# Optimization experiments

Hardware: AMD Instinct MI355X
Metric: run time of the kernel (lower is better)

## Reference

```python
import jax, jax.numpy as jnp
import numpy as np

N = 100000   # nodes
E = 1200000  # edges
C = 64       # in_channels
H = 64       # hidden_channels
OUT = 10     # out_channels
G = 128      # graphs in batch
L = 3        # num_conv_layers
EPS = 1e-5   # BatchNorm eps


def batchnorm(x, g, b):
    # training-mode BatchNorm1d: biased batch stats over the node/graph axis
    mu = x.mean(axis=0)
    var = x.var(axis=0)
    return (x - mu) * jax.lax.rsqrt(var + EPS) * g + b


def _gcn_norm(edge_index):
    # add self-loops (weight 1) then symmetric normalization deg^-1/2 * w * deg^-1/2
    loop = jnp.arange(N)
    src = jnp.concatenate([edge_index[0], loop])
    dst = jnp.concatenate([edge_index[1], loop])
    w = jnp.ones((E + N,), jnp.float32)
    deg = jax.ops.segment_sum(w, src, num_segments=N)
    dis = jnp.where(deg > 0, jax.lax.rsqrt(deg), 0.0)
    norm = dis[src] * w * dis[dst]
    return src, dst, norm


def gcn_conv(h, W, b, src, dst, norm):
    # linear transform -> gather source features -> edge-normalize -> scatter-add to dst
    hw = h @ W
    msg = norm[:, None] * hw[src]          # [E+N, H]
    return jax.ops.segment_sum(msg, dst, num_segments=N) + b


def setup_inputs() -> dict:
    key = jax.random.key(0)
    ks = jax.random.split(key, 8)
    s = 0.1
    return {
        'x': jax.random.normal(ks[0], (N, C), jnp.float32),
        'edge_index': jax.random.randint(ks[1], (2, E), 0, N),
        'batch_idx': jnp.sort(jax.random.randint(ks[2], (N,), 0, G)),
        # BN params initialized as in the module: weight=1, bias=1e-4
        'bn_feat_g': jnp.ones((C,), jnp.float32),
        'bn_feat_b': jnp.full((C,), 1e-4, jnp.float32),
        'W_feat': jax.random.normal(ks[3], (C, H), jnp.float32) * s,  # conv_feat (gfn=True -> pure linear)
        'b_feat': jnp.zeros((H,), jnp.float32),
        'conv_bn_g': jnp.ones((L, H), jnp.float32),
        'conv_bn_b': jnp.full((L, H), 1e-4, jnp.float32),
        'conv_W': jax.random.normal(ks[4], (L, H, H), jnp.float32) * s,
        'conv_b': jnp.zeros((L, H), jnp.float32),
        'bn_fc_g': jnp.ones((H,), jnp.float32),
        'bn_fc_b': jnp.full((H,), 1e-4, jnp.float32),
        'W_fc': jax.random.normal(ks[5], (H, H), jnp.float32) * s,
        'b_fc': jnp.zeros((H,), jnp.float32),
        'bn_hid_g': jnp.ones((H,), jnp.float32),
        'bn_hid_b': jnp.full((H,), 1e-4, jnp.float32),
        'W_cls': jax.random.normal(ks[6], (H, OUT), jnp.float32) * s,
        'b_cls': jnp.zeros((OUT,), jnp.float32),
    }


def reference(x, edge_index, batch_idx, bn_feat_g, bn_feat_b, W_feat, b_feat,
              conv_bn_g, conv_bn_b, conv_W, conv_b, bn_fc_g, bn_fc_b, W_fc, b_fc,
              bn_hid_g, bn_hid_b, W_cls, b_cls):
    src, dst, norm = _gcn_norm(edge_index)
    # forward_BNConvReLU, residual=False, gating=None, xg=None, dropout=0
    h = batchnorm(x, bn_feat_g, bn_feat_b)
    h = jax.nn.relu(h @ W_feat + b_feat)           # conv_feat: gfn=True => linear only
    for i in range(L):
        h_ = batchnorm(h, conv_bn_g[i], conv_bn_b[i])
        h = jax.nn.relu(gcn_conv(h_, conv_W[i], conv_b[i], src, dst, norm))
    hg = jax.ops.segment_sum(h, batch_idx, num_segments=G)  # global_add_pool -> [G, H]
    h_ = batchnorm(hg, bn_fc_g, bn_fc_b)
    hg = jax.nn.relu(h_ @ W_fc + b_fc)
    hg = batchnorm(hg, bn_hid_g, bn_hid_b)
    logits = hg @ W_cls + b_cls
    return jax.nn.log_softmax(logits, axis=-1)
```

## Files before the change

### kernel.cpp

```cpp
#include <hip/hip_runtime.h>
#include <hip/hip_fp16.h>

#define N_NODES 100000
#define N_EDGES 1200000
#define GRAPHS 128
#define EPSBN 1e-5f
#define NSHARD 8
#define SH_NODES 12500


__global__ __launch_bounds__(256) void k_build(const int* __restrict__ src,
                                               const int* __restrict__ dst,
                                               int* __restrict__ cnt,
                                               int* __restrict__ deg,
                                               int* __restrict__ ecsr) {
    int shard = blockIdx.x & (NSHARD - 1);
    int lo = shard * SH_NODES, hi = lo + SH_NODES;
    int t = threadIdx.x;
    for (int e = (blockIdx.x >> 3) * 256 + t; e < N_EDGES; e += 65536) {
        int s = __builtin_nontemporal_load(&src[e]);
        int d = __builtin_nontemporal_load(&dst[e]);
        if (s >= lo && s < hi) atomicAdd(&deg[s], 1);
        if (d >= lo && d < hi) {
            int p = atomicAdd(&cnt[d], 1);
            ecsr[(d << 6) + p] = s;
        }
    }
}

__global__ __launch_bounds__(256) void k_dis(const int* __restrict__ deg,
                                             float* __restrict__ dis) {
    int i = blockIdx.x * 256 + threadIdx.x;
    if (i < N_NODES) dis[i] = rsqrtf((float)deg[i] + 1.0f);
}


__global__ __launch_bounds__(256) void k_sigma(const float* __restrict__ dis,
                                               const int* __restrict__ cnt,
                                               const int* __restrict__ ecsr,
                                               float* __restrict__ sigma) {
    int lane = threadIdx.x & 63;
    int wid = threadIdx.x >> 6;
    for (int node = blockIdx.x * 4 + wid; node < N_NODES; node += gridDim.x * 4) {
        int m = cnt[node];
        int sraw = ecsr[(node << 6) + lane];
        float dd = dis[node];
        int sL = (lane < m) ? sraw : 0;
        float v = (lane < m) ? dis[sL] : 0.f;
#pragma unroll
        for (int d = 1; d <= 32; d <<= 1) v += __shfl_xor(v, d, 64);
        if (lane == 0) sigma[node] = dd * (v + dd);
    }
}


__global__ __launch_bounds__(256) void k_stats(const float* __restrict__ x,
                                               float* __restrict__ sums) {
    const float4* x4 = (const float4*)x;
    int t = threadIdx.x;
    int q = t & 15, rg = t >> 4;
    float4 s = {0.f, 0.f, 0.f, 0.f}, s2 = {0.f, 0.f, 0.f, 0.f};
    for (int r = blockIdx.x * 16 + rg; r < N_NODES; r += gridDim.x * 16) {
        float4 v = x4[r * 16 + q];
        s.x += v.x; s.y += v.y; s.z += v.z; s.w += v.w;
        s2.x += v.x * v.x; s2.y += v.y * v.y; s2.z += v.z * v.z; s2.w += v.w * v.w;
    }
    __shared__ float red[2][16][64];
    red[0][rg][q * 4 + 0] = s.x;  red[0][rg][q * 4 + 1] = s.y;
    red[0][rg][q * 4 + 2] = s.z;  red[0][rg][q * 4 + 3] = s.w;
    red[1][rg][q * 4 + 0] = s2.x; red[1][rg][q * 4 + 1] = s2.y;
    red[1][rg][q * 4 + 2] = s2.z; red[1][rg][q * 4 + 3] = s2.w;
    __syncthreads();
    if (t < 64) {
        float a = 0.f, b = 0.f;
#pragma unroll
        for (int k = 0; k < 16; k++) { a += red[0][k][t]; b += red[1][k][t]; }
        atomicAdd(&sums[t], a);
        atomicAdd(&sums[64 + t], b);
    }
}


__global__ __launch_bounds__(256) void k_fold(const float* __restrict__ sums, const float* __restrict__ g,
                       const float* __restrict__ b, const float* __restrict__ W,
                       const float* __restrict__ bias_in, int has_bias,
                       float* __restrict__ Wout, float* __restrict__ bout) {
    __shared__ float a[64], cc[64];
    int t = threadIdx.x;
    if (t < 64) {
        float mu = sums[t] * (1.0f / N_NODES);
        float var = sums[64 + t] * (1.0f / N_NODES) - mu * mu;
        float av = g[t] * rsqrtf(var + EPSBN);
        a[t] = av;
        cc[t] = b[t] - mu * av;
    }
    __syncthreads();
    for (int i = t; i < 4096; i += 256) Wout[i] = a[i >> 6] * W[i];
    if (t < 64) {
        float acc = has_bias ? bias_in[t] : 0.0f;
        for (int k = 0; k < 64; k++) acc += cc[k] * W[k * 64 + t];
        bout[t] = acc;
    }
}


__global__ __launch_bounds__(256, 4) void k_gemm2(const float* __restrict__ X, const float* __restrict__ W,
                        const float* __restrict__ bias, const float* __restrict__ dis,
                        __half* __restrict__ U,
                        float* __restrict__ sums, int do_stats) {
    int t = threadIdx.x;
    int j = t & 63;
    int rg = t >> 6;
    __shared__ float wlds[64][64];
    __shared__ float xs[16][64];
    for (int i = t; i < 4096; i += 256) wlds[i >> 6][i & 63] = W[i];
    float bj = bias[j];
    __syncthreads();
    float s_sum = 0.f, s_sq = 0.f;
    for (int base = blockIdx.x * 16; base < N_NODES; base += gridDim.x * 16) {
        ((float4*)xs)[t] = ((const float4*)(X + base * 64))[t];
        int r0 = rg * 4;
        float a0 = bj, a1 = bj, a2 = bj, a3 = bj;
        const float4* x0 = (const float4*)xs[r0 + 0];
        const float4* x1 = (const float4*)xs[r0 + 1];
        const float4* x2 = (const float4*)xs[r0 + 2];
        const float4* x3 = (const float4*)xs[r0 + 3];
#pragma unroll
        for (int q4 = 0; q4 < 16; q4++) {
            float w0 = wlds[q4 * 4 + 0][j], w1 = wlds[q4 * 4 + 1][j];
            float w2 = wlds[q4 * 4 + 2][j], w3 = wlds[q4 * 4 + 3][j];
            float4 v0 = x0[q4]; a0 += v0.x * w0 + v0.y * w1 + v0.z * w2 + v0.w * w3;
            float4 v1 = x1[q4]; a1 += v1.x * w0 + v1.y * w1 + v1.z * w2 + v1.w * w3;
            float4 v2 = x2[q4]; a2 += v2.x * w0 + v2.y * w1 + v2.z * w2 + v2.w * w3;
            float4 v3 = x3[q4]; a3 += v3.x * w0 + v3.y * w1 + v3.z * w2 + v3.w * w3;
        }
        a0 = fmaxf(a0, 0.f); a1 = fmaxf(a1, 0.f);
        a2 = fmaxf(a2, 0.f); a3 = fmaxf(a3, 0.f);
        int nb = base + r0;
        U[(nb + 0) * 64 + j] = __float2half_rn(a0 * dis[nb + 0]);
        U[(nb + 1) * 64 + j] = __float2half_rn(a1 * dis[nb + 1]);
        U[(nb + 2) * 64 + j] = __float2half_rn(a2 * dis[nb + 2]);
        U[(nb + 3) * 64 + j] = __float2half_rn(a3 * dis[nb + 3]);
        if (do_stats) {
            s_sum += a0 + a1 + a2 + a3;
            s_sq += a0 * a0 + a1 * a1 + a2 * a2 + a3 * a3;
        }
    }
    if (do_stats) {
        __syncthreads();
        xs[rg][j] = s_sum;
        xs[4 + rg][j] = s_sq;
        __syncthreads();
        if (t < 64) {
            atomicAdd(&sums[t], xs[0][t] + xs[1][t] + xs[2][t] + xs[3][t]);
            atomicAdd(&sums[64 + t], xs[4][t] + xs[5][t] + xs[6][t] + xs[7][t]);
        }
    }
}


__global__ __launch_bounds__(256, 4) void k_aggemm(const __half* __restrict__ u,
                        const float* __restrict__ dis, const float* __restrict__ sigma,
                        const int* __restrict__ cnt, const int* __restrict__ ecsr,
                        const float* __restrict__ sums_in, const float* __restrict__ bng,
                        const float* __restrict__ bnb,
                        const float* __restrict__ W, const float* __restrict__ bias,
                        __half* __restrict__ uout, float* __restrict__ hout, int last,
                        float* __restrict__ sums_out, int do_stats) {
    const __half2* u2 = (const __half2*)u;
    int t = threadIdx.x;
    int j = t & 63;
    int wid = t >> 6;
    int g = j >> 5, c = j & 31;
    __shared__ float wlds[64][64];
    __shared__ float xs[16][64];
    if (t < 64) {
        float mu = sums_in[t] * (1.0f / N_NODES);
        float var = sums_in[64 + t] * (1.0f / N_NODES) - mu * mu;
        float av = bng[t] * rsqrtf(var + EPSBN);
        xs[0][t] = av;
        xs[1][t] = bnb[t] - mu * av;
    }
    __syncthreads();
    for (int i = t; i < 4096; i += 256) wlds[i >> 6][i & 63] = W[i] * xs[0][i >> 6];
    float cb = 0.f;
#pragma unroll 8
    for (int q = 0; q < 64; q++) cb += xs[1][q] * W[q * 64 + j];
    float bj = bias[j];
    __syncthreads();
    float s_sum = 0.f, s_sq = 0.f;
    for (int base = blockIdx.x * 16; base < N_NODES; base += gridDim.x * 16) {
        int r0 = wid * 4;
        int nb = base + r0;
        int mm[4], srw[4];
        float dvals[4], svals[4];
        __half2 selfs[4];
#pragma unroll
        for (int r = 0; r < 4; r++) {
            mm[r] = cnt[nb + r];
            srw[r] = ecsr[((nb + r) << 6) + j];
            dvals[r] = dis[nb + r];
            svals[r] = sigma[nb + r];
            selfs[r] = u2[(nb + r) * 32 + c];
        }
#pragma unroll
        for (int rp = 0; rp < 2; rp++) {
            int ra = 2 * rp, rb = 2 * rp + 1;
            int ma = mm[ra], mb = mm[rb];
            int sLa = (j < ma) ? srw[ra] : 0;
            int sLb = (j < mb) ? srw[rb] : 0;
            float axa = 0.f, aya = 0.f, axb = 0.f, ayb = 0.f;
#pragma unroll
            for (int k = 0; k < 8; k++) {
                int e = 2 * k + g;
                int sEa = __shfl(sLa, e, 64);
                int sEb = __shfl(sLb, e, 64);
                float wa = (e < ma) ? 1.0f : 0.0f;
                float wb = (e < mb) ? 1.0f : 0.0f;
                float2 fa = __half22float2(u2[sEa * 32 + c]);
                float2 fb = __half22float2(u2[sEb * 32 + c]);
                axa += wa * fa.x; aya += wa * fa.y;
                axb += wb * fb.x; ayb += wb * fb.y;
            }
            if (ma > 16) {
                for (int e = 16 + g; e < ma; e += 2) {
                    int sE = __shfl(sLa, e, 64);
                    float2 f = __half22float2(u2[sE * 32 + c]);
                    axa += f.x; aya += f.y;
                }
            }
            if (mb > 16) {
                for (int e = 16 + g; e < mb; e += 2) {
                    int sE = __shfl(sLb, e, 64);
                    float2 f = __half22float2(u2[sE * 32 + c]);
                    axb += f.x; ayb += f.y;
                }
            }
            axa += __shfl_xor(axa, 32, 64); aya += __shfl_xor(aya, 32, 64);
            axb += __shfl_xor(axb, 32, 64); ayb += __shfl_xor(ayb, 32, 64);
            if (g == 0) {
                float2 sfa = __half22float2(selfs[ra]);
                float2 sfb = __half22float2(selfs[rb]);
                float da = dvals[ra], db = dvals[rb];
                xs[r0 + ra][2 * c + 0] = da * (axa + sfa.x);
                xs[r0 + ra][2 * c + 1] = da * (aya + sfa.y);
                xs[r0 + rb][2 * c + 0] = db * (axb + sfb.x);
                xs[r0 + rb][2 * c + 1] = db * (ayb + sfb.y);
            }
        }
        float a0 = bj + svals[0] * cb, a1 = bj + svals[1] * cb;
        float a2 = bj + svals[2] * cb, a3 = bj + svals[3] * cb;
        const float4* x0 = (const float4*)xs[r0 + 0];
        const float4* x1 = (const float4*)xs[r0 + 1];
        const float4* x2 = (const float4*)xs[r0 + 2];
        const float4* x3 = (const float4*)xs[r0 + 3];
#pragma unroll
        for (int q4 = 0; q4 < 16; q4++) {
            float w0 = wlds[q4 * 4 + 0][j], w1 = wlds[q4 * 4 + 1][j];
            float w2 = wlds[q4 * 4 + 2][j], w3 = wlds[q4 * 4 + 3][j];
            float4 v0 = x0[q4]; a0 += v0.x * w0 + v0.y * w1 + v0.z * w2 + v0.w * w3;
            float4 v1 = x1[q4]; a1 += v1.x * w0 + v1.y * w1 + v1.z * w2 + v1.w * w3;
            float4 v2 = x2[q4]; a2 += v2.x * w0 + v2.y * w1 + v2.z * w2 + v2.w * w3;
            float4 v3 = x3[q4]; a3 += v3.x * w0 + v3.y * w1 + v3.z * w2 + v3.w * w3;
        }
        a0 = fmaxf(a0, 0.f); a1 = fmaxf(a1, 0.f);
        a2 = fmaxf(a2, 0.f); a3 = fmaxf(a3, 0.f);
        if (last) {
            hout[(nb + 0) * 64 + j] = a0;
            hout[(nb + 1) * 64 + j] = a1;
            hout[(nb + 2) * 64 + j] = a2;
            hout[(nb + 3) * 64 + j] = a3;
        } else {
            uout[(nb + 0) * 64 + j] = __float2half_rn(a0 * dvals[0]);
            uout[(nb + 1) * 64 + j] = __float2half_rn(a1 * dvals[1]);
            uout[(nb + 2) * 64 + j] = __float2half_rn(a2 * dvals[2]);
            uout[(nb + 3) * 64 + j] = __float2half_rn(a3 * dvals[3]);
        }
        if (do_stats) {
            s_sum += a0 + a1 + a2 + a3;
            s_sq += a0 * a0 + a1 * a1 + a2 * a2 + a3 * a3;
        }
    }
    if (do_stats) {
        __syncthreads();
        xs[wid][j] = s_sum;
        xs[4 + wid][j] = s_sq;
        __syncthreads();
        if (t < 64) {
            atomicAdd(&sums_out[t], xs[0][t] + xs[1][t] + xs[2][t] + xs[3][t]);
            atomicAdd(&sums_out[64 + t], xs[4][t] + xs[5][t] + xs[6][t] + xs[7][t]);
        }
    }
}


__global__ __launch_bounds__(256) void k_pool(const float* __restrict__ h, const int* __restrict__ batch,
                       float* __restrict__ hg) {
    int g = blockIdx.x >> 2, q3 = blockIdx.x & 3;
    int lo = 0, hi = N_NODES;
    while (lo < hi) { int m = (lo + hi) >> 1; if (batch[m] < g) lo = m + 1; else hi = m; }
    int start = lo;
    lo = start; hi = N_NODES;
    while (lo < hi) { int m = (lo + hi) >> 1; if (batch[m] < g + 1) lo = m + 1; else hi = m; }
    int end = lo;
    int len = end - start;
    int c0 = start + ((len * q3) >> 2);
    int c1 = start + ((len * (q3 + 1)) >> 2);
    int c = threadIdx.x & 63, rg = threadIdx.x >> 6;
    float s = 0.f;
    for (int r = c0 + rg; r < c1; r += 4) s += h[r * 64 + c];
    __shared__ float ls[4][64];
    ls[rg][c] = s;
    __syncthreads();
    if (rg == 0) atomicAdd(&hg[g * 64 + c], ls[0][c] + ls[1][c] + ls[2][c] + ls[3][c]);
}


__global__ __launch_bounds__(512) void k_tail(const float* __restrict__ hg_in,
                       const float* __restrict__ g1, const float* __restrict__ b1,
                       const float* __restrict__ Wfc, const float* __restrict__ bfc,
                       const float* __restrict__ g2, const float* __restrict__ b2,
                       const float* __restrict__ Wcls, const float* __restrict__ bcls,
                       float* __restrict__ out) {
    __shared__ float hgn[8192];
    __shared__ float h2[8192];
    __shared__ float red[2][8][64];
    __shared__ float a[64], cc[64];
    __shared__ float Wc[640];
    __shared__ float logits[1280];
    __shared__ float lse[128];
    int t = threadIdx.x;
    int j = t & 63;
    int w = t >> 6;

    {
        float su = 0.f, sq = 0.f;
#pragma unroll
        for (int gg = 0; gg < 16; gg++) {
            float v = hg_in[(w * 16 + gg) * 64 + j];
            su += v; sq += v * v;
        }
        red[0][w][j] = su; red[1][w][j] = sq;
    }
    for (int i = t; i < 640; i += 512) Wc[i] = Wcls[i];
    __syncthreads();
    if (t < 64) {
        float su = 0.f, sq = 0.f;
#pragma unroll
        for (int k = 0; k < 8; k++) { su += red[0][k][t]; sq += red[1][k][t]; }
        float mu = su * (1.f / 128.f);
        float var = sq * (1.f / 128.f) - mu * mu;
        float av = g1[t] * rsqrtf(var + EPSBN);
        a[t] = av; cc[t] = b1[t] - mu * av;
    }
    __syncthreads();
    for (int i = t; i < 8192; i += 512) hgn[i] = hg_in[i] * a[i & 63] + cc[i & 63];

    float wreg[64];
#pragma unroll
    for (int q = 0; q < 64; q++) wreg[q] = Wfc[q * 64 + j];
    float bj = bfc[j];
    __syncthreads();

    float acc[16];
#pragma unroll
    for (int r = 0; r < 16; r++) acc[r] = bj;
    const float4* hgn4 = (const float4*)hgn;
#pragma unroll
    for (int q4 = 0; q4 < 16; q4++) {
#pragma unroll
        for (int r = 0; r < 16; r++) {
            float4 hv = hgn4[(w * 16 + r) * 16 + q4];
            acc[r] += hv.x * wreg[q4 * 4 + 0] + hv.y * wreg[q4 * 4 + 1]
                    + hv.z * wreg[q4 * 4 + 2] + hv.w * wreg[q4 * 4 + 3];
        }
    }
    float s = 0.f, s2 = 0.f;
#pragma unroll
    for (int r = 0; r < 16; r++) {
        float v = fmaxf(acc[r], 0.f);
        h2[(w * 16 + r) * 64 + j] = v;
        s += v; s2 += v * v;
    }
    red[0][w][j] = s; red[1][w][j] = s2;
    __syncthreads();

    if (t < 64) {
        float su = 0.f, sq = 0.f;
#pragma unroll
        for (int k = 0; k < 8; k++) { su += red[0][k][t]; sq += red[1][k][t]; }
        float mu = su * (1.f / 128.f);
        float var = sq * (1.f / 128.f) - mu * mu;
        float av = g2[t] * rsqrtf(var + EPSBN);
        a[t] = av; cc[t] = b2[t] - mu * av;
    }
    __syncthreads();
    for (int i = t; i < 8192; i += 512) h2[i] = h2[i] * a[i & 63] + cc[i & 63];
    __syncthreads();

    for (int idx = t; idx < 1280; idx += 512) {
        int row = idx / 10, o = idx - row * 10;
        float v = bcls[o];
#pragma unroll
        for (int q = 0; q < 64; q++) v += h2[row * 64 + q] * Wc[q * 10 + o];
        logits[idx] = v;
    }
    __syncthreads();
    if (t < 128) {
        float mx = -1e30f;
#pragma unroll
        for (int o = 0; o < 10; o++) mx = fmaxf(mx, logits[t * 10 + o]);
        float se = 0.f;
#pragma unroll
        for (int o = 0; o < 10; o++) se += expf(logits[t * 10 + o] - mx);
        lse[t] = mx + logf(se);
    }
    __syncthreads();
    for (int idx = t; idx < 1280; idx += 512) out[idx] = logits[idx] - lse[idx / 10];
}


extern "C" void kernel_launch(void* const* d_in, const int* in_sizes, int n_in,
                              void* d_out, int out_size, void* d_ws, size_t ws_size,
                              hipStream_t stream) {
    const float* x         = (const float*)d_in[0];
    const int*   ei        = (const int*)  d_in[1];
    const int*   batch     = (const int*)  d_in[2];
    const float* bn_feat_g = (const float*)d_in[3];
    const float* bn_feat_b = (const float*)d_in[4];
    const float* W_feat    = (const float*)d_in[5];
    const float* b_feat    = (const float*)d_in[6];
    const float* conv_bn_g = (const float*)d_in[7];
    const float* conv_bn_b = (const float*)d_in[8];
    const float* conv_W    = (const float*)d_in[9];
    const float* conv_b    = (const float*)d_in[10];
    const float* bn_fc_g   = (const float*)d_in[11];
    const float* bn_fc_b   = (const float*)d_in[12];
    const float* W_fc      = (const float*)d_in[13];
    const float* b_fc      = (const float*)d_in[14];
    const float* bn_hid_g  = (const float*)d_in[15];
    const float* bn_hid_b  = (const float*)d_in[16];
    const float* W_cls     = (const float*)d_in[17];
    const float* b_cls     = (const float*)d_in[18];
    float* out = (float*)d_out;

    float* ws    = (float*)d_ws;
    float* hbuf  = ws;
    __half* u_a  = (__half*)(ws + 6400000);
    __half* u_b  = (__half*)(ws + 9600000);
    float* dis   = ws + 12800000;
    float* sigma = ws + 12900000;
    float* Wt    = ws + 13000000;
    float* bt    = Wt + 4096;
    float* hg    = bt + 64;
    float* sums  = hg + 8192;
    int*   cnt   = (int*)(sums + 640);
    int*   ecsr  = cnt + 100000;
    int*   deg   = (int*)u_b;

    float* sx = sums;
    float* s0 = sums + 128;
    float* s1 = sums + 256;
    float* s2 = sums + 384;

    const int* srcp = ei;
    const int* dstp = ei + N_EDGES;

    hipMemsetAsync(hg, 0, (8192 + 640 + 100000) * sizeof(float), stream);
    hipMemsetAsync(deg, 0, 100000 * sizeof(int), stream);

    k_build<<<2048, 256, 0, stream>>>(srcp, dstp, cnt, deg, ecsr);
    k_dis<<<(N_NODES + 255) / 256, 256, 0, stream>>>(deg, dis);
    k_sigma<<<1024, 256, 0, stream>>>(dis, cnt, ecsr, sigma);

    k_stats<<<512, 256, 0, stream>>>(x, sx);
    k_fold<<<1, 256, 0, stream>>>(sx, bn_feat_g, bn_feat_b, W_feat, b_feat, 1, Wt, bt);
    k_gemm2<<<2048, 256, 0, stream>>>(x, Wt, bt, dis, u_a, s0, 1);

    k_aggemm<<<2048, 256, 0, stream>>>(u_a, dis, sigma, cnt, ecsr,
                                       s0, conv_bn_g + 0, conv_bn_b + 0,
                                       conv_W + 0, conv_b + 0,
                                       u_b, nullptr, 0, s1, 1);
    k_aggemm<<<2048, 256, 0, stream>>>(u_b, dis, sigma, cnt, ecsr,
                                       s1, conv_bn_g + 64, conv_bn_b + 64,
                                       conv_W + 4096, conv_b + 64,
                                       u_a, nullptr, 0, s2, 1);
    k_aggemm<<<2048, 256, 0, stream>>>(u_a, dis, sigma, cnt, ecsr,
                                       s2, conv_bn_g + 128, conv_bn_b + 128,
                                       conv_W + 8192, conv_b + 128,
                                       nullptr, hbuf, 1, nullptr, 0);

    k_pool<<<4 * GRAPHS, 256, 0, stream>>>(hbuf, batch, hg);
    k_tail<<<1, 512, 0, stream>>>(hg, bn_fc_g, bn_fc_b, W_fc, b_fc,
                                  bn_hid_g, bn_hid_b, W_cls, b_cls, out);
}
```

Measured before the change: 542.6 us.

## Merge independent preprocessing kernels by block-range dispatch and widen unrolled gather loop

Fuses the CSR build with the input BN stats, the deg^-1/2 computation with the BN weight fold, and the sigma computation with the first GEMM. Each pair runs in one launch, with block index ranges picking the role, so the number of launches drops from six to three and independent work can overlap. It also raises the unrolled edge loop in the aggregation kernel from 16 to 32 edges, so fewer nodes fall into the slow tail loop. The cost is more masked loads for low-degree nodes and possible load imbalance between the different roles inside a grid.

```diff
diff --git a/kernel.cpp b/kernel.cpp
--- a/kernel.cpp
+++ b/kernel.cpp
@@ -9,144 +9,126 @@
 #define SH_NODES 12500
 
 
-__global__ __launch_bounds__(256) void k_build(const int* __restrict__ src,
-                                               const int* __restrict__ dst,
-                                               int* __restrict__ cnt,
-                                               int* __restrict__ deg,
-                                               int* __restrict__ ecsr) {
-    int shard = blockIdx.x & (NSHARD - 1);
-    int lo = shard * SH_NODES, hi = lo + SH_NODES;
+__global__ __launch_bounds__(256) void k_build_stats(const int* __restrict__ src,
+                                                     const int* __restrict__ dst,
+                                                     int* __restrict__ cnt,
+                                                     int* __restrict__ deg,
+                                                     int* __restrict__ ecsr,
+                                                     const float* __restrict__ x,
+                                                     float* __restrict__ sums) {
     int t = threadIdx.x;
-    for (int e = (blockIdx.x >> 3) * 256 + t; e < N_EDGES; e += 65536) {
-        int s = __builtin_nontemporal_load(&src[e]);
-        int d = __builtin_nontemporal_load(&dst[e]);
-        if (s >= lo && s < hi) atomicAdd(&deg[s], 1);
-        if (d >= lo && d < hi) {
-            int p = atomicAdd(&cnt[d], 1);
-            ecsr[(d << 6) + p] = s;
-        }
-    }
-}
-
-__global__ __launch_bounds__(256) void k_dis(const int* __restrict__ deg,
-                                             float* __restrict__ dis) {
-    int i = blockIdx.x * 256 + threadIdx.x;
-    if (i < N_NODES) dis[i] = rsqrtf((float)deg[i] + 1.0f);
-}
-
-
-__global__ __launch_bounds__(256) void k_sigma(const float* __restrict__ dis,
-                                               const int* __restrict__ cnt,
-                                               const int* __restrict__ ecsr,
-                                               float* __restrict__ sigma) {
-    int lane = threadIdx.x & 63;
-    int wid = threadIdx.x >> 6;
-    for (int node = blockIdx.x * 4 + wid; node < N_NODES; node += gridDim.x * 4) {
-        int m = cnt[node];
-        int sraw = ecsr[(node << 6) + lane];
-        float dd = dis[node];
-        int sL = (lane < m) ? sraw : 0;
-        float v = (lane < m) ? dis[sL] : 0.f;
-#pragma unroll
-        for (int d = 1; d <= 32; d <<= 1) v += __shfl_xor(v, d, 64);
-        if (lane == 0) sigma[node] = dd * (v + dd);
-    }
-}
-
-
-__global__ __launch_bounds__(256) void k_stats(const float* __restrict__ x,
-                                               float* __restrict__ sums) {
-    const float4* x4 = (const float4*)x;
+    if (blockIdx.x < 2048) {
+        int shard = blockIdx.x & (NSHARD - 1);
+        int lo = shard * SH_NODES, hi = lo + SH_NODES;
+        for (int e = (blockIdx.x >> 3) * 256 + t; e < N_EDGES; e += 65536) {
+            int s = __builtin_nontemporal_load(&src[e]);
+            int d = __builtin_nontemporal_load(&dst[e]);
+            if (s >= lo && s < hi) atomicAdd(&deg[s], 1);
+            if (d >= lo && d < hi) {
+                int p = atomicAdd(&cnt[d], 1);
+                ecsr[(d << 6) + p] = s;
+            }
+        }
+    } else {
+        int bid = blockIdx.x - 2048;
+        const float4* x4 = (const float4*)x;
+        int q = t & 15, rg = t >> 4;
+        float4 s = {0.f, 0.f, 0.f, 0.f}, s2 = {0.f, 0.f, 0.f, 0.f};
+        for (int r = bid * 16 + rg; r < N_NODES; r += 512 * 16) {
+            float4 v = x4[r * 16 + q];
+            s.x += v.x; s.y += v.y; s.z += v.z; s.w += v.w;
+            s2.x += v.x * v.x; s2.y += v.y * v.y; s2.z += v.z * v.z; s2.w += v.w * v.w;
+        }
+        __shared__ float red[2][16][64];
+        red[0][rg][q * 4 + 0] = s.x;  red[0][rg][q * 4 + 1] = s.y;
+        red[0][rg][q * 4 + 2] = s.z;  red[0][rg][q * 4 + 3] = s.w;
+        red[1][rg][q * 4 + 0] = s2.x; red[1][rg][q * 4 + 1] = s2.y;
+        red[1][rg][q * 4 + 2] = s2.z; red[1][rg][q * 4 + 3] = s2.w;
+        __syncthreads();
+        if (t < 64) {
+            float a = 0.f, b = 0.f;
+#pragma unroll
+            for (int k = 0; k < 16; k++) { a += red[0][k][t]; b += red[1][k][t]; }
+            atomicAdd(&sums[t], a);
+            atomicAdd(&sums[64 + t], b);
+        }
+    }
+}
+
+
+__global__ __launch_bounds__(256) void k_dis_fold(const int* __restrict__ deg,
+                       float* __restrict__ dis,
+                       const float* __restrict__ sums, const float* __restrict__ g,
+                       const float* __restrict__ b, const float* __restrict__ W,
+                       const float* __restrict__ bias_in,
+                       float* __restrict__ Wout, float* __restrict__ bout) {
     int t = threadIdx.x;
-    int q = t & 15, rg = t >> 4;
-    float4 s = {0.f, 0.f, 0.f, 0.f}, s2 = {0.f, 0.f, 0.f, 0.f};
-    for (int r = blockIdx.x * 16 + rg; r < N_NODES; r += gridDim.x * 16) {
-        float4 v = x4[r * 16 + q];
-        s.x += v.x; s.y += v.y; s.z += v.z; s.w += v.w;
-        s2.x += v.x * v.x; s2.y += v.y * v.y; s2.z += v.z * v.z; s2.w += v.w * v.w;
-    }
-    __shared__ float red[2][16][64];
-    red[0][rg][q * 4 + 0] = s.x;  red[0][rg][q * 4 + 1] = s.y;
-    red[0][rg][q * 4 + 2] = s.z;  red[0][rg][q * 4 + 3] = s.w;
-    red[1][rg][q * 4 + 0] = s2.x; red[1][rg][q * 4 + 1] = s2.y;
-    red[1][rg][q * 4 + 2] = s2.z; red[1][rg][q * 4 + 3] = s2.w;
-    __syncthreads();
-    if (t < 64) {
-        float a = 0.f, b = 0.f;
-#pragma unroll
-        for (int k = 0; k < 16; k++) { a += red[0][k][t]; b += red[1][k][t]; }
-        atomicAdd(&sums[t], a);
-        atomicAdd(&sums[64 + t], b);
-    }
-}
-
-
-__global__ __launch_bounds__(256) void k_fold(const float* __restrict__ sums, const float* __restrict__ g,
-                       const float* __restrict__ b, const float* __restrict__ W,
-                       const float* __restrict__ bias_in, int has_bias,
-                       float* __restrict__ Wout, float* __restrict__ bout) {
-    __shared__ float a[64], cc[64];
-    int t = threadIdx.x;
-    if (t < 64) {
-        float mu = sums[t] * (1.0f / N_NODES);
-        float var = sums[64 + t] * (1.0f / N_NODES) - mu * mu;
-        float av = g[t] * rsqrtf(var + EPSBN);
-        a[t] = av;
-        cc[t] = b[t] - mu * av;
-    }
-    __syncthreads();
-    for (int i = t; i < 4096; i += 256) Wout[i] = a[i >> 6] * W[i];
-    if (t < 64) {
-        float acc = has_bias ? bias_in[t] : 0.0f;
-        for (int k = 0; k < 64; k++) acc += cc[k] * W[k * 64 + t];
-        bout[t] = acc;
-    }
-}
-
-
-__global__ __launch_bounds__(256, 4) void k_gemm2(const float* __restrict__ X, const float* __restrict__ W,
+    if (blockIdx.x < 391) {
+        int i = blockIdx.x * 256 + t;
+        if (i < N_NODES) dis[i] = rsqrtf((float)deg[i] + 1.0f);
+    } else {
+        __shared__ float a[64], cc[64];
+        if (t < 64) {
+            float mu = sums[t] * (1.0f / N_NODES);
+            float var = sums[64 + t] * (1.0f / N_NODES) - mu * mu;
+            float av = g[t] * rsqrtf(var + EPSBN);
+            a[t] = av;
+            cc[t] = b[t] - mu * av;
+        }
+        __syncthreads();
+        for (int i = t; i < 4096; i += 256) Wout[i] = a[i >> 6] * W[i];
+        if (t < 64) {
+            float acc = bias_in[t];
+            for (int k = 0; k < 64; k++) acc += cc[k] * W[k * 64 + t];
+            bout[t] = acc;
+        }
+    }
+}
+
+
+__global__ __launch_bounds__(256, 4) void k_sigma_gemm2(const float* __restrict__ X,
+                        const float* __restrict__ W,
                         const float* __restrict__ bias, const float* __restrict__ dis,
-                        __half* __restrict__ U,
-                        float* __restrict__ sums, int do_stats) {
-    int t = threadIdx.x;
-    int j = t & 63;
-    int rg = t >> 6;
+                        __half* __restrict__ U, float* __restrict__ sums,
+                        const int* __restrict__ cnt, const int* __restrict__ ecsr,
+                        float* __restrict__ sigma) {
     __shared__ float wlds[64][64];
     __shared__ float xs[16][64];
-    for (int i = t; i < 4096; i += 256) wlds[i >> 6][i & 63] = W[i];
-    float bj = bias[j];
-    __syncthreads();
-    float s_sum = 0.f, s_sq = 0.f;
-    for (int base = blockIdx.x * 16; base < N_NODES; base += gridDim.x * 16) {
-        ((float4*)xs)[t] = ((const float4*)(X + base * 64))[t];
-        int r0 = rg * 4;
-        float a0 = bj, a1 = bj, a2 = bj, a3 = bj;
-        const float4* x0 = (const float4*)xs[r0 + 0];
-        const float4* x1 = (const float4*)xs[r0 + 1];
-        const float4* x2 = (const float4*)xs[r0 + 2];
-        const float4* x3 = (const float4*)xs[r0 + 3];
-#pragma unroll
-        for (int q4 = 0; q4 < 16; q4++) {
-            float w0 = wlds[q4 * 4 + 0][j], w1 = wlds[q4 * 4 + 1][j];
-            float w2 = wlds[q4 * 4 + 2][j], w3 = wlds[q4 * 4 + 3][j];
-            float4 v0 = x0[q4]; a0 += v0.x * w0 + v0.y * w1 + v0.z * w2 + v0.w * w3;
-            float4 v1 = x1[q4]; a1 += v1.x * w0 + v1.y * w1 + v1.z * w2 + v1.w * w3;
-            float4 v2 = x2[q4]; a2 += v2.x * w0 + v2.y * w1 + v2.z * w2 + v2.w * w3;
-            float4 v3 = x3[q4]; a3 += v3.x * w0 + v3.y * w1 + v3.z * w2 + v3.w * w3;
-        }
-        a0 = fmaxf(a0, 0.f); a1 = fmaxf(a1, 0.f);
-        a2 = fmaxf(a2, 0.f); a3 = fmaxf(a3, 0.f);
-        int nb = base + r0;
-        U[(nb + 0) * 64 + j] = __float2half_rn(a0 * dis[nb + 0]);
-        U[(nb + 1) * 64 + j] = __float2half_rn(a1 * dis[nb + 1]);
-        U[(nb + 2) * 64 + j] = __float2half_rn(a2 * dis[nb + 2]);
-        U[(nb + 3) * 64 + j] = __float2half_rn(a3 * dis[nb + 3]);
-        if (do_stats) {
+    int t = threadIdx.x;
+    if (blockIdx.x < 2048) {
+        int j = t & 63;
+        int rg = t >> 6;
+        for (int i = t; i < 4096; i += 256) wlds[i >> 6][i & 63] = W[i];
+        float bj = bias[j];
+        __syncthreads();
+        float s_sum = 0.f, s_sq = 0.f;
+        for (int base = blockIdx.x * 16; base < N_NODES; base += 2048 * 16) {
+            ((float4*)xs)[t] = ((const float4*)(X + base * 64))[t];
+            int r0 = rg * 4;
+            float a0 = bj, a1 = bj, a2 = bj, a3 = bj;
+            const float4* x0 = (const float4*)xs[r0 + 0];
+            const float4* x1 = (const float4*)xs[r0 + 1];
+            const float4* x2 = (const float4*)xs[r0 + 2];
+            const float4* x3 = (const float4*)xs[r0 + 3];
+#pragma unroll
+            for (int q4 = 0; q4 < 16; q4++) {
+                float w0 = wlds[q4 * 4 + 0][j], w1 = wlds[q4 * 4 + 1][j];
+                float w2 = wlds[q4 * 4 + 2][j], w3 = wlds[q4 * 4 + 3][j];
+                float4 v0 = x0[q4]; a0 += v0.x * w0 + v0.y * w1 + v0.z * w2 + v0.w * w3;
+                float4 v1 = x1[q4]; a1 += v1.x * w0 + v1.y * w1 + v1.z * w2 + v1.w * w3;
+                float4 v2 = x2[q4]; a2 += v2.x * w0 + v2.y * w1 + v2.z * w2 + v2.w * w3;
+                float4 v3 = x3[q4]; a3 += v3.x * w0 + v3.y * w1 + v3.z * w2 + v3.w * w3;
+            }
+            a0 = fmaxf(a0, 0.f); a1 = fmaxf(a1, 0.f);
+            a2 = fmaxf(a2, 0.f); a3 = fmaxf(a3, 0.f);
+            int nb = base + r0;
+            U[(nb + 0) * 64 + j] = __float2half_rn(a0 * dis[nb + 0]);
+            U[(nb + 1) * 64 + j] = __float2half_rn(a1 * dis[nb + 1]);
+            U[(nb + 2) * 64 + j] = __float2half_rn(a2 * dis[nb + 2]);
+            U[(nb + 3) * 64 + j] = __float2half_rn(a3 * dis[nb + 3]);
             s_sum += a0 + a1 + a2 + a3;
             s_sq += a0 * a0 + a1 * a1 + a2 * a2 + a3 * a3;
         }
-    }
-    if (do_stats) {
         __syncthreads();
         xs[rg][j] = s_sum;
         xs[4 + rg][j] = s_sq;
@@ -154,6 +136,20 @@
         if (t < 64) {
             atomicAdd(&sums[t], xs[0][t] + xs[1][t] + xs[2][t] + xs[3][t]);
             atomicAdd(&sums[64 + t], xs[4][t] + xs[5][t] + xs[6][t] + xs[7][t]);
+        }
+    } else {
+        int bid = blockIdx.x - 2048;
+        int lane = t & 63;
+        int wid = t >> 6;
+        for (int node = bid * 4 + wid; node < N_NODES; node += 1024 * 4) {
+            int m = cnt[node];
+            int sraw = ecsr[(node << 6) + lane];
+            float dd = dis[node];
+            int sL = (lane < m) ? sraw : 0;
+            float v = (lane < m) ? dis[sL] : 0.f;
+#pragma unroll
+            for (int d = 1; d <= 32; d <<= 1) v += __shfl_xor(v, d, 64);
+            if (lane == 0) sigma[node] = dd * (v + dd);
         }
     }
 }
@@ -211,7 +207,7 @@
             int sLb = (j < mb) ? srw[rb] : 0;
             float axa = 0.f, aya = 0.f, axb = 0.f, ayb = 0.f;
 #pragma unroll
-            for (int k = 0; k < 8; k++) {
+            for (int k = 0; k < 16; k++) {
                 int e = 2 * k + g;
                 int sEa = __shfl(sLa, e, 64);
                 int sEb = __shfl(sLb, e, 64);
@@ -222,15 +218,15 @@
                 axa += wa * fa.x; aya += wa * fa.y;
                 axb += wb * fb.x; ayb += wb * fb.y;
             }
-            if (ma > 16) {
-                for (int e = 16 + g; e < ma; e += 2) {
+            if (ma > 32) {
+                for (int e = 32 + g; e < ma; e += 2) {
                     int sE = __shfl(sLa, e, 64);
                     float2 f = __half22float2(u2[sE * 32 + c]);
                     axa += f.x; aya += f.y;
                 }
             }
-            if (mb > 16) {
-                for (int e = 16 + g; e < mb; e += 2) {
+            if (mb > 32) {
+                for (int e = 32 + g; e < mb; e += 2) {
                     int sE = __shfl(sLb, e, 64);
                     float2 f = __half22float2(u2[sE * 32 + c]);
                     axb += f.x; ayb += f.y;
@@ -469,13 +465,10 @@
     hipMemsetAsync(hg, 0, (8192 + 640 + 100000) * sizeof(float), stream);
     hipMemsetAsync(deg, 0, 100000 * sizeof(int), stream);
 
-    k_build<<<2048, 256, 0, stream>>>(srcp, dstp, cnt, deg, ecsr);
-    k_dis<<<(N_NODES + 255) / 256, 256, 0, stream>>>(deg, dis);
-    k_sigma<<<1024, 256, 0, stream>>>(dis, cnt, ecsr, sigma);
-
-    k_stats<<<512, 256, 0, stream>>>(x, sx);
-    k_fold<<<1, 256, 0, stream>>>(sx, bn_feat_g, bn_feat_b, W_feat, b_feat, 1, Wt, bt);
-    k_gemm2<<<2048, 256, 0, stream>>>(x, Wt, bt, dis, u_a, s0, 1);
+    k_build_stats<<<2560, 256, 0, stream>>>(srcp, dstp, cnt, deg, ecsr, x, sx);
+    k_dis_fold<<<392, 256, 0, stream>>>(deg, dis, sx, bn_feat_g, bn_feat_b,
+                                        W_feat, b_feat, Wt, bt);
+    k_sigma_gemm2<<<3072, 256, 0, stream>>>(x, Wt, bt, dis, u_a, s0, cnt, ecsr, sigma);
 
     k_aggemm<<<2048, 256, 0, stream>>>(u_a, dis, sigma, cnt, ecsr,
                                        s0, conv_bn_g + 0, conv_bn_b + 0,
```

Result: slower. 568.0 us (+4.7%).
